# Kernel optimization log

Hardware: AMD Instinct MI355X
Metric: run time of the kernel (lower is better)

Reference implementation:

```python
import jax, jax.numpy as jnp
import numpy as np

HEADS = 16  # per module init; all heads share the same weights -> identical outputs


def setup_inputs() -> dict:
    key = jax.random.key(0)
    k1, k2, k3, k4 = jax.random.split(key, 4)
    B, S, E, HD = 8, 2048, 1024, 64  # embed_size=1024, heads=16, head_dim=64
    x = jax.random.normal(k1, (B, S, E), dtype=jnp.float32)
    Wq = jax.random.normal(k2, (HD, E), dtype=jnp.float32) * (E ** -0.5)
    Wk = jax.random.normal(k3, (HD, E), dtype=jnp.float32) * (E ** -0.5)
    Wv = jax.random.normal(k4, (HD, E), dtype=jnp.float32) * (E ** -0.5)
    return {"x": x, "Wq": Wq, "Wk": Wk, "Wv": Wv}


def reference(x, Wq, Wk, Wv):
    # Linear(embed, head_dim, bias=False): y = x @ W.T
    q = jnp.einsum('bse,de->bsd', x, Wq)  # [B,S,64]
    k = jnp.einsum('bse,de->bsd', x, Wk)
    v = jnp.einsum('bse,de->bsd', x, Wv)
    # scores [b, i(query), k(key)] -- NO scaling (scaled_factor unused in source)
    scores = jnp.einsum('bij,bkj->bik', q, k)
    # nn.Softmax(dim=1): normalize over the QUERY axis (axis=1), faithful quirk
    attn = jax.nn.softmax(scores, axis=1)
    out = jnp.matmul(attn, v)  # [B,S,64]
    # Per-head loop reuses identical weights -> concat == tile across heads
    return jnp.tile(out, (1, 1, HEADS))  # [B,S,1024]
```

## Files before the change

### kernel.cpp

```cpp
#include <hip/hip_runtime.h>

#define BATCH 8
#define SEQ   2048
#define EMB   1024
#define HD    64
#define HEADS 16
#define BS    (BATCH * SEQ)
#define LOG2E 1.4426950408889634f

typedef _Float16 half8 __attribute__((ext_vector_type(8)));
typedef _Float16 half4 __attribute__((ext_vector_type(4)));
typedef float    f32x4 __attribute__((ext_vector_type(4)));

__device__ __forceinline__ float fexp2(float x) {
#if __has_builtin(__builtin_amdgcn_exp2f)
    return __builtin_amdgcn_exp2f(x);
#else
    return exp2f(x);
#endif
}

__device__ __forceinline__ float frcp(float x) {
#if __has_builtin(__builtin_amdgcn_rcpf)
    return __builtin_amdgcn_rcpf(x);
#else
    return 1.0f / x;
#endif
}

__device__ __forceinline__ void dma16(void* lds_base, const void* gsrc) {
    __builtin_amdgcn_global_load_lds(
        (const __attribute__((address_space(1))) unsigned int*)gsrc,
        (__attribute__((address_space(3))) unsigned int*)lds_base, 16, 0, 0);
}

__global__ __launch_bounds__(256) void wcvt_kernel(
    const float* __restrict__ Wq, const float* __restrict__ Wk,
    const float* __restrict__ Wv, _Float16* __restrict__ Wh)
{
    const int m = blockIdx.y;
    const float* src = (m == 0) ? Wq : (m == 1) ? Wk : Wv;
    const float scale = (m == 0) ? LOG2E : 1.0f;
    const int idx = (blockIdx.x * 256 + threadIdx.x) * 8;
    float4 f0 = *(const float4*)(src + idx);
    float4 f1 = *(const float4*)(src + idx + 4);
    half8 h;
    h[0] = (_Float16)(f0.x * scale); h[1] = (_Float16)(f0.y * scale);
    h[2] = (_Float16)(f0.z * scale); h[3] = (_Float16)(f0.w * scale);
    h[4] = (_Float16)(f1.x * scale); h[5] = (_Float16)(f1.y * scale);
    h[6] = (_Float16)(f1.z * scale); h[7] = (_Float16)(f1.w * scale);
    *(half8*)(Wh + (size_t)m * 65536 + idx) = h;
}

__global__ __launch_bounds__(512) void qkv_kernel(
    const float* __restrict__ x, const _Float16* __restrict__ Wh,
    _Float16* __restrict__ qh, _Float16* __restrict__ kh, _Float16* __restrict__ vpk)
{
    __shared__ __align__(16) char arena[65536];
    const int t = threadIdx.x, lane = t & 63, wave = t >> 6;
    const int l15 = lane & 15, quad = lane >> 4;
    const int strip = wave & 1, grp = wave >> 1;
    const int row0 = blockIdx.x * 32;

    auto issue = [&](int buf, int k0) {
        #pragma unroll
        for (int jj = 0; jj < 4; ++jj) {
            const int j = wave * 4 + jj;
            if (j < 8) {
                const int row = j * 4 + (lane >> 4);
                const int logi = (lane & 15) ^ (row & 15);
                dma16((float*)(arena + buf * 8192) + j * 256,
                      x + (size_t)(row0 + row) * EMB + k0 + logi * 4);
            } else {
                const int jw = j - 8;
                const int dd = jw * 8 + (lane >> 3);
                const int logi = (lane & 7) ^ (dd & 7);
                dma16((_Float16*)(arena + 16384 + buf * 24576) + jw * 512,
                      Wh + (size_t)(dd >> 6) * 65536 + (size_t)(dd & 63) * EMB
                         + k0 + logi * 8);
            }
        }
    };

    issue(0, 0);
    __syncthreads();

    f32x4 acc[3] = {};
    const int xrow = strip * 16 + l15;
    for (int it = 0; it < 16; ++it) {
        const int buf = it & 1;
        if (it + 1 < 16) issue(buf ^ 1, (it + 1) * 64);
        const float* xb = (const float*)(arena + buf * 8192);
        const _Float16* wb = (const _Float16*)(arena + 16384 + buf * 24576);
        half8 a[2];
        #pragma unroll
        for (int kc = 0; kc < 2; ++kc) {
            const int s0 = kc * 8 + quad * 2;
            f32x4 u0 = *(const f32x4*)(xb + xrow * 64 + ((s0    ) ^ (l15 & 15)) * 4);
            f32x4 u1 = *(const f32x4*)(xb + xrow * 64 + ((s0 + 1) ^ (l15 & 15)) * 4);
            a[kc][0] = (_Float16)u0[0]; a[kc][1] = (_Float16)u0[1];
            a[kc][2] = (_Float16)u0[2]; a[kc][3] = (_Float16)u0[3];
            a[kc][4] = (_Float16)u1[0]; a[kc][5] = (_Float16)u1[1];
            a[kc][6] = (_Float16)u1[2]; a[kc][7] = (_Float16)u1[3];
        }
        #pragma unroll
        for (int j = 0; j < 3; ++j) {
            const int dd = (grp * 3 + j) * 16 + l15;
            #pragma unroll
            for (int kc = 0; kc < 2; ++kc) {
                half8 bfr = *(const half8*)(wb + dd * 64
                              + (((kc * 4 + quad) ^ (l15 & 7)) * 8));
                acc[j] = __builtin_amdgcn_mfma_f32_16x16x32_f16(a[kc], bfr, acc[j], 0, 0, 0);
            }
        }
        __syncthreads();
    }

    #pragma unroll
    for (int j = 0; j < 3; ++j) {
        const int c = grp * 3 + j, m = c >> 2, n = c & 3;
        if (m < 2) {
            _Float16* __restrict__ dst = (m == 0) ? qh : kh;
            #pragma unroll
            for (int r = 0; r < 4; ++r)
                dst[(size_t)(row0 + strip * 16 + quad * 4 + r) * HD + n * 16 + l15] =
                    (_Float16)acc[j][r];
        } else {
            const int rg = row0 + strip * 16 + quad * 4;
            const int b = rg >> 11, s = rg & 2047;
            half4 h;
            h[0] = (_Float16)acc[j][0]; h[1] = (_Float16)acc[j][1];
            h[2] = (_Float16)acc[j][2]; h[3] = (_Float16)acc[j][3];
            *(half4*)(vpk + (((size_t)b * 256 + (s >> 3)) * 64 + n * 16 + l15) * 8
                          + (s & 7)) = h;
        }
    }
}

__global__ __launch_bounds__(256, 4) void stats_kernel(
    const _Float16* __restrict__ qh, const _Float16* __restrict__ kh,
    float* __restrict__ l_part)
{
    __shared__ float red[4][32];
    const int t = threadIdx.x, lane = t & 63, wave = t >> 6;
    const int l15 = lane & 15, quad = lane >> 4;
    const int b = blockIdx.y, c0 = blockIdx.x * 32, z = blockIdx.z;

    half8 ka[2][2];
    #pragma unroll
    for (int kt = 0; kt < 2; ++kt) {
        const _Float16* kp = kh + ((size_t)b * SEQ + c0 + kt * 16 + l15) * HD + quad * 8;
        ka[kt][0] = *(const half8*)(kp);
        ka[kt][1] = *(const half8*)(kp + 32);
    }

    const _Float16* qp0 = qh + ((size_t)b * SEQ + z * 1024 + wave * 16 + l15) * HD + quad * 8;
    float csum[2][4] = {};
    for (int it = 0; it < 16; ++it) {
        const _Float16* qp = qp0 + (size_t)it * 64 * HD;
        half8 bq0 = *(const half8*)(qp);
        half8 bq1 = *(const half8*)(qp + 32);
        f32x4 s0 = {}, s1 = {};
        s0 = __builtin_amdgcn_mfma_f32_16x16x32_f16(ka[0][0], bq0, s0, 0, 0, 0);
        s0 = __builtin_amdgcn_mfma_f32_16x16x32_f16(ka[0][1], bq1, s0, 0, 0, 0);
        s1 = __builtin_amdgcn_mfma_f32_16x16x32_f16(ka[1][0], bq0, s1, 0, 0, 0);
        s1 = __builtin_amdgcn_mfma_f32_16x16x32_f16(ka[1][1], bq1, s1, 0, 0, 0);
        #pragma unroll
        for (int r = 0; r < 4; ++r) {
            csum[0][r] += fexp2(s0[r]);
            csum[1][r] += fexp2(s1[r]);
        }
    }
    #pragma unroll
    for (int kt = 0; kt < 2; ++kt)
        #pragma unroll
        for (int r = 0; r < 4; ++r) {
            csum[kt][r] += __shfl_xor(csum[kt][r], 1);
            csum[kt][r] += __shfl_xor(csum[kt][r], 2);
            csum[kt][r] += __shfl_xor(csum[kt][r], 4);
            csum[kt][r] += __shfl_xor(csum[kt][r], 8);
        }
    if (l15 == 0) {
        #pragma unroll
        for (int kt = 0; kt < 2; ++kt)
            #pragma unroll
            for (int r = 0; r < 4; ++r)
                red[wave][kt * 16 + quad * 4 + r] = csum[kt][r];
    }
    __syncthreads();
    if (t < 32)
        l_part[(size_t)z * BS + (size_t)b * SEQ + c0 + t] =
            red[0][t] + red[1][t] + red[2][t] + red[3][t];
}

__global__ __launch_bounds__(256, 4) void out_kernel(
    const _Float16* __restrict__ qh, const _Float16* __restrict__ kh,
    const _Float16* __restrict__ vpk, const float* __restrict__ l_part,
    float* __restrict__ opart)
{
    __shared__ __align__(16) char arena[22528];
    const int t = threadIdx.x, lane = t & 63, wave = t >> 6;
    const int l15 = lane & 15, quad = lane >> 4;
    const int rw = wave & 1, kw = wave >> 1;
    const int b = blockIdx.y, r0 = blockIdx.x * 32, z = blockIdx.z;
    const int kbase = z * 1024;

    half8 aq[2];
    {
        const _Float16* qp = qh + ((size_t)b * SEQ + r0 + rw * 16 + l15) * HD + quad * 8;
        aq[0] = *(const half8*)(qp);
        aq[1] = *(const half8*)(qp + 32);
    }

    const float* lp = l_part + (size_t)b * SEQ;
    _Float16* psb = (_Float16*)(arena) + wave * 640;
    f32x4 oacc[4] = {};
    for (int it = 0; it < 16; ++it) {
        const int c0 = kbase + it * 64;
        f32x4 s[2] = {};
        float li[2];
        #pragma unroll
        for (int ct = 0; ct < 2; ++ct) {
            const int key = c0 + kw * 32 + ct * 16 + l15;
            const _Float16* kp = kh + ((size_t)b * SEQ + key) * HD + quad * 8;
            half8 kf0 = *(const half8*)(kp);
            half8 kf1 = *(const half8*)(kp + 32);
            s[ct] = __builtin_amdgcn_mfma_f32_16x16x32_f16(aq[0], kf0, s[ct], 0, 0, 0);
            s[ct] = __builtin_amdgcn_mfma_f32_16x16x32_f16(aq[1], kf1, s[ct], 0, 0, 0);
            li[ct] = frcp(lp[key] + lp[BS + key]);
        }
        #pragma unroll
        for (int ct = 0; ct < 2; ++ct)
            #pragma unroll
            for (int r = 0; r < 4; ++r)
                psb[(quad * 4 + r) * 40 + ct * 16 + l15] =
                    (_Float16)(fexp2(s[ct][r]) * li[ct]);
        half8 pa = *(const half8*)(psb + l15 * 40 + quad * 8);
        const _Float16* vbase = vpk
            + ((size_t)b * 256 + (c0 >> 3) + kw * 4 + quad) * 512;
        #pragma unroll
        for (int n = 0; n < 4; ++n) {
            half8 vf = *(const half8*)(vbase + (n * 16 + l15) * 8);
            oacc[n] = __builtin_amdgcn_mfma_f32_16x16x32_f16(pa, vf, oacc[n], 0, 0, 0);
        }
    }

    float* red = (float*)(arena + 5120);
    float* fin = (float*)(arena + 13824);
    if (kw == 1) {
        #pragma unroll
        for (int n = 0; n < 4; ++n)
            #pragma unroll
            for (int r = 0; r < 4; ++r)
                red[(rw * 16 + quad * 4 + r) * 68 + n * 16 + l15] = oacc[n][r];
    }
    __syncthreads();
    if (kw == 0) {
        #pragma unroll
        for (int n = 0; n < 4; ++n)
            #pragma unroll
            for (int r = 0; r < 4; ++r)
                fin[(rw * 16 + quad * 4 + r) * 68 + n * 16 + l15] =
                    oacc[n][r] + red[(rw * 16 + quad * 4 + r) * 68 + n * 16 + l15];
    }
    __syncthreads();

    const int row = t >> 3, s8 = t & 7;
    float4 u0 = *(float4*)(fin + row * 68 + s8 * 8);
    float4 u1 = *(float4*)(fin + row * 68 + s8 * 8 + 4);
    float* dst = opart + (size_t)z * ((size_t)BS * HD)
               + ((size_t)b * SEQ + r0 + row) * HD + s8 * 8;
    *(float4*)(dst)     = u0;
    *(float4*)(dst + 4) = u1;
}

__global__ __launch_bounds__(256) void bcast_kernel(
    const float* __restrict__ opart, float* __restrict__ out)
{
    const int row = blockIdx.x;
    const int t = threadIdx.x;
    const int d = (t * 4) & 63;
    const float* o0 = opart + (size_t)row * HD + d;
    const float* o1 = o0 + (size_t)BS * HD;
    float4 a = *(const float4*)o0;
    float4 c = *(const float4*)o1;
    float4 s;
    s.x = a.x + c.x; s.y = a.y + c.y; s.z = a.z + c.z; s.w = a.w + c.w;
    *(float4*)(out + (size_t)row * (HD * HEADS) + t * 4) = s;
}

extern "C" void kernel_launch(void* const* d_in, const int* in_sizes, int n_in,
                              void* d_out, int out_size, void* d_ws, size_t ws_size,
                              hipStream_t stream)
{
    const float* x  = (const float*)d_in[0];
    const float* Wq = (const float*)d_in[1];
    const float* Wk = (const float*)d_in[2];
    const float* Wv = (const float*)d_in[3];
    float* out = (float*)d_out;

    const size_t N = (size_t)BATCH * SEQ * HD;
    _Float16* qh  = (_Float16*)d_ws;
    _Float16* kh  = qh + N;
    _Float16* vpk = kh + N;
    _Float16* Wh  = vpk + N;
    float* l_part = (float*)(Wh + 196608);
    float* opart  = l_part + 2 * BS;

    wcvt_kernel <<<dim3(32, 3),    256, 0, stream>>>(Wq, Wk, Wv, Wh);
    qkv_kernel  <<<dim3(512),      512, 0, stream>>>(x, Wh, qh, kh, vpk);
    stats_kernel<<<dim3(64, 8, 2), 256, 0, stream>>>(qh, kh, l_part);
    out_kernel  <<<dim3(64, 8, 2), 256, 0, stream>>>(qh, kh, vpk, l_part, opart);
    bcast_kernel<<<dim3(BS),       256, 0, stream>>>(opart, out);
}
```

Before: 193.7 us.

## Fuse broadcast into out_kernel, drop key split, software-pipeline K/V/Q loads

The out_kernel no longer splits the key range across two z-blocks. Each block now covers all 2048 keys and writes the 16 head copies straight to the output, which removes the opart buffer and the separate bcast kernel. Both stats_kernel and out_kernel get two-stage register double buffering of their global loads, with two LDS P buffers per wave, so memory latency overlaps with MFMA work. The cost is half as many out_kernel blocks, which may reduce parallelism, plus higher register pressure that could lower occupancy.

After: 193.3 us. About the same (-0.2%).

```diff
diff --git a/kernel.cpp b/kernel.cpp
--- a/kernel.cpp
+++ b/kernel.cpp
@@ -156,10 +156,8 @@
 
     const _Float16* qp0 = qh + ((size_t)b * SEQ + z * 1024 + wave * 16 + l15) * HD + quad * 8;
     float csum[2][4] = {};
-    for (int it = 0; it < 16; ++it) {
-        const _Float16* qp = qp0 + (size_t)it * 64 * HD;
-        half8 bq0 = *(const half8*)(qp);
-        half8 bq1 = *(const half8*)(qp + 32);
+
+    auto accum = [&](half8 bq0, half8 bq1) {
         f32x4 s0 = {}, s1 = {};
         s0 = __builtin_amdgcn_mfma_f32_16x16x32_f16(ka[0][0], bq0, s0, 0, 0, 0);
         s0 = __builtin_amdgcn_mfma_f32_16x16x32_f16(ka[0][1], bq1, s0, 0, 0, 0);
@@ -170,7 +168,23 @@
             csum[0][r] += fexp2(s0[r]);
             csum[1][r] += fexp2(s1[r]);
         }
-    }
+    };
+
+    half8 bqA0 = *(const half8*)(qp0);
+    half8 bqA1 = *(const half8*)(qp0 + 32);
+    for (int it = 0; it < 16; it += 2) {
+        const _Float16* qpB = qp0 + (size_t)(it + 1) * 64 * HD;
+        half8 bqB0 = *(const half8*)(qpB);
+        half8 bqB1 = *(const half8*)(qpB + 32);
+        accum(bqA0, bqA1);
+        if (it + 2 < 16) {
+            const _Float16* qpA = qp0 + (size_t)(it + 2) * 64 * HD;
+            bqA0 = *(const half8*)(qpA);
+            bqA1 = *(const half8*)(qpA + 32);
+        }
+        accum(bqB0, bqB1);
+    }
+
     #pragma unroll
     for (int kt = 0; kt < 2; ++kt)
         #pragma unroll
@@ -196,14 +210,13 @@
 __global__ __launch_bounds__(256, 4) void out_kernel(
     const _Float16* __restrict__ qh, const _Float16* __restrict__ kh,
     const _Float16* __restrict__ vpk, const float* __restrict__ l_part,
-    float* __restrict__ opart)
-{
-    __shared__ __align__(16) char arena[22528];
+    float* __restrict__ out)
+{
+    __shared__ __align__(16) char arena[27648];
     const int t = threadIdx.x, lane = t & 63, wave = t >> 6;
     const int l15 = lane & 15, quad = lane >> 4;
     const int rw = wave & 1, kw = wave >> 1;
-    const int b = blockIdx.y, r0 = blockIdx.x * 32, z = blockIdx.z;
-    const int kbase = z * 1024;
+    const int b = blockIdx.y, r0 = blockIdx.x * 32;
 
     half8 aq[2];
     {
@@ -213,40 +226,65 @@
     }
 
     const float* lp = l_part + (size_t)b * SEQ;
-    _Float16* psb = (_Float16*)(arena) + wave * 640;
-    f32x4 oacc[4] = {};
-    for (int it = 0; it < 16; ++it) {
-        const int c0 = kbase + it * 64;
-        f32x4 s[2] = {};
-        float li[2];
+    _Float16* psA = (_Float16*)(arena) + wave * 1280;
+    _Float16* psB = psA + 640;
+
+    auto loadRegs = [&](int it, half8 (&kf)[2][2], half8 (&vf)[4],
+                        float (&l0)[2], float (&l1)[2]) {
+        const int c0 = it * 64;
         #pragma unroll
         for (int ct = 0; ct < 2; ++ct) {
             const int key = c0 + kw * 32 + ct * 16 + l15;
             const _Float16* kp = kh + ((size_t)b * SEQ + key) * HD + quad * 8;
-            half8 kf0 = *(const half8*)(kp);
-            half8 kf1 = *(const half8*)(kp + 32);
-            s[ct] = __builtin_amdgcn_mfma_f32_16x16x32_f16(aq[0], kf0, s[ct], 0, 0, 0);
-            s[ct] = __builtin_amdgcn_mfma_f32_16x16x32_f16(aq[1], kf1, s[ct], 0, 0, 0);
-            li[ct] = frcp(lp[key] + lp[BS + key]);
-        }
-        #pragma unroll
-        for (int ct = 0; ct < 2; ++ct)
-            #pragma unroll
-            for (int r = 0; r < 4; ++r)
-                psb[(quad * 4 + r) * 40 + ct * 16 + l15] =
-                    (_Float16)(fexp2(s[ct][r]) * li[ct]);
-        half8 pa = *(const half8*)(psb + l15 * 40 + quad * 8);
+            kf[ct][0] = *(const half8*)(kp);
+            kf[ct][1] = *(const half8*)(kp + 32);
+            l0[ct] = lp[key];
+            l1[ct] = lp[BS + key];
+        }
         const _Float16* vbase = vpk
             + ((size_t)b * 256 + (c0 >> 3) + kw * 4 + quad) * 512;
         #pragma unroll
-        for (int n = 0; n < 4; ++n) {
-            half8 vf = *(const half8*)(vbase + (n * 16 + l15) * 8);
-            oacc[n] = __builtin_amdgcn_mfma_f32_16x16x32_f16(pa, vf, oacc[n], 0, 0, 0);
-        }
-    }
-
-    float* red = (float*)(arena + 5120);
-    float* fin = (float*)(arena + 13824);
+        for (int n = 0; n < 4; ++n)
+            vf[n] = *(const half8*)(vbase + (n * 16 + l15) * 8);
+    };
+
+    f32x4 oacc[4] = {};
+    auto compute = [&](const half8 (&kf)[2][2], const half8 (&vf)[4],
+                       const float (&l0)[2], const float (&l1)[2],
+                       _Float16* psb) {
+        f32x4 s[2] = {};
+        #pragma unroll
+        for (int ct = 0; ct < 2; ++ct) {
+            s[ct] = __builtin_amdgcn_mfma_f32_16x16x32_f16(aq[0], kf[ct][0], s[ct], 0, 0, 0);
+            s[ct] = __builtin_amdgcn_mfma_f32_16x16x32_f16(aq[1], kf[ct][1], s[ct], 0, 0, 0);
+        }
+        #pragma unroll
+        for (int ct = 0; ct < 2; ++ct) {
+            const float li = frcp(l0[ct] + l1[ct]);
+            #pragma unroll
+            for (int r = 0; r < 4; ++r)
+                psb[(quad * 4 + r) * 40 + ct * 16 + l15] =
+                    (_Float16)(fexp2(s[ct][r]) * li);
+        }
+        half8 pa = *(const half8*)(psb + l15 * 40 + quad * 8);
+        #pragma unroll
+        for (int n = 0; n < 4; ++n)
+            oacc[n] = __builtin_amdgcn_mfma_f32_16x16x32_f16(pa, vf[n], oacc[n], 0, 0, 0);
+    };
+
+    half8 kfA[2][2], vfA[4], kfB[2][2], vfB[4];
+    float l0A[2], l1A[2], l0B[2], l1B[2];
+    loadRegs(0, kfA, vfA, l0A, l1A);
+    for (int it = 0; it < 32; it += 2) {
+        loadRegs(it + 1, kfB, vfB, l0B, l1B);
+        compute(kfA, vfA, l0A, l1A, psA);
+        if (it + 2 < 32)
+            loadRegs(it + 2, kfA, vfA, l0A, l1A);
+        compute(kfB, vfB, l0B, l1B, psB);
+    }
+
+    float* red = (float*)(arena + 10240);
+    float* fin = (float*)(arena + 18944);
     if (kw == 1) {
         #pragma unroll
         for (int n = 0; n < 4; ++n)
@@ -268,25 +306,12 @@
     const int row = t >> 3, s8 = t & 7;
     float4 u0 = *(float4*)(fin + row * 68 + s8 * 8);
     float4 u1 = *(float4*)(fin + row * 68 + s8 * 8 + 4);
-    float* dst = opart + (size_t)z * ((size_t)BS * HD)
-               + ((size_t)b * SEQ + r0 + row) * HD + s8 * 8;
-    *(float4*)(dst)     = u0;
-    *(float4*)(dst + 4) = u1;
-}
-
-__global__ __launch_bounds__(256) void bcast_kernel(
-    const float* __restrict__ opart, float* __restrict__ out)
-{
-    const int row = blockIdx.x;
-    const int t = threadIdx.x;
-    const int d = (t * 4) & 63;
-    const float* o0 = opart + (size_t)row * HD + d;
-    const float* o1 = o0 + (size_t)BS * HD;
-    float4 a = *(const float4*)o0;
-    float4 c = *(const float4*)o1;
-    float4 s;
-    s.x = a.x + c.x; s.y = a.y + c.y; s.z = a.z + c.z; s.w = a.w + c.w;
-    *(float4*)(out + (size_t)row * (HD * HEADS) + t * 4) = s;
+    size_t base = ((size_t)b * SEQ + r0 + row) * (HD * HEADS);
+    #pragma unroll
+    for (int h = 0; h < HEADS; ++h) {
+        *(float4*)&out[base + h * HD + s8 * 8]     = u0;
+        *(float4*)&out[base + h * HD + s8 * 8 + 4] = u1;
+    }
 }
 
 extern "C" void kernel_launch(void* const* d_in, const int* in_sizes, int n_in,
@@ -305,11 +330,9 @@
     _Float16* vpk = kh + N;
     _Float16* Wh  = vpk + N;
     float* l_part = (float*)(Wh + 196608);
-    float* opart  = l_part + 2 * BS;
 
     wcvt_kernel <<<dim3(32, 3),    256, 0, stream>>>(Wq, Wk, Wv, Wh);
     qkv_kernel  <<<dim3(512),      512, 0, stream>>>(x, Wh, qh, kh, vpk);
     stats_kernel<<<dim3(64, 8, 2), 256, 0, stream>>>(qh, kh, l_part);
-    out_kernel  <<<dim3(64, 8, 2), 256, 0, stream>>>(qh, kh, vpk, l_part, opart);
-    bcast_kernel<<<dim3(BS),       256, 0, stream>>>(opart, out);
-}
+    out_kernel  <<<dim3(64, 8),    256, 0, stream>>>(qh, kh, vpk, l_part, out);
+}
```
